# Optimization experiments

Hardware: AMD Instinct MI355X
Metric: run time of the kernel (lower is better)

The kernel has to match this reference:

```python
import jax, jax.numpy as jnp
import numpy as np

N, E, D, H, L = 50000, 800000, 64, 4, 2
DH = D // H


def layer_norm(h, g, b, eps=1e-5):
    mu = h.mean(-1, keepdims=True)
    var = ((h - mu) ** 2).mean(-1, keepdims=True)
    return (h - mu) / jnp.sqrt(var + eps) * g + b


def setup_inputs() -> dict:
    key = jax.random.key(0)
    ks = jax.random.split(key, 16)
    s = 1.0 / np.sqrt(D)
    inp = {
        "x": jax.random.normal(ks[0], (N, D), jnp.float32),
        "edge_attr": jax.random.normal(ks[1], (E, D), jnp.float32),
        "edge_index": jax.random.randint(ks[2], (2, E), 0, N, jnp.int64),
        "WQ": jax.random.normal(ks[3], (L, D, D), jnp.float32) * s,
        "WK": jax.random.normal(ks[4], (L, D, D), jnp.float32) * s,
        "WE": jax.random.normal(ks[5], (L, D, D), jnp.float32) * s,
        "WV": jax.random.normal(ks[6], (L, D, D), jnp.float32) * s,
        "WO": jax.random.normal(ks[7], (L, D, D), jnp.float32) * s,
        "bO": jnp.zeros((L, D), jnp.float32),
        "ln1_g": jnp.ones((L, D), jnp.float32),
        "ln1_b": jnp.zeros((L, D), jnp.float32),
        "W1": jax.random.normal(ks[8], (L, D, 2 * D), jnp.float32) * s,
        "b1": jnp.zeros((L, 2 * D), jnp.float32),
        "W2": jax.random.normal(ks[9], (L, 2 * D, D), jnp.float32) * (1.0 / np.sqrt(2 * D)),
        "b2": jnp.zeros((L, D), jnp.float32),
        "ln2_g": jnp.ones((L, D), jnp.float32),
        "ln2_b": jnp.zeros((L, D), jnp.float32),
    }
    return inp


def exphormer_layer(h, edge_attr, src, dst, p):
    (wq, wk, we, wv, wo, bo, g1, be1, w1, b1, w2, b2, g2, be2) = p
    n = h.shape[0]
    Qh = (h @ wq).reshape(n, H, DH)
    Kh = (h @ wk).reshape(n, H, DH)
    Vh = (h @ wv).reshape(n, H, DH)
    Eh = (edge_attr @ we).reshape(-1, H, DH)
    # per-edge score: sum over head_dim of K[src]*Q[dst]*E / sqrt(DH)
    s = jnp.sum(Kh[src] * Qh[dst] * Eh, axis=-1, keepdims=True) / np.sqrt(DH)
    score = jnp.exp(jnp.clip(s, -5.0, 5.0))  # [E, H, 1]
    msg = Vh[src] * score                     # [E, H, DH]
    wV = jax.ops.segment_sum(msg, dst, num_segments=n)    # [N, H, DH]
    Z = jax.ops.segment_sum(score, dst, num_segments=n)   # [N, H, 1]
    h_attn = (wV / (Z + 1e-6)).reshape(n, D)
    h1 = layer_norm(h + (h_attn @ wo + bo), g1, be1)
    ffn = jax.nn.relu(h1 @ w1 + b1) @ w2 + b2
    return layer_norm(h1 + ffn, g2, be2)


def reference(x, edge_attr, edge_index, WQ, WK, WE, WV, WO, bO, ln1_g, ln1_b,
              W1, b1, W2, b2, ln2_g, ln2_b):
    src = edge_index[0]
    dst = edge_index[1]
    h = x
    for l in range(L):
        p = (WQ[l], WK[l], WE[l], WV[l], WO[l], bO[l], ln1_g[l], ln1_b[l],
             W1[l], b1[l], W2[l], b2[l], ln2_g[l], ln2_b[l])
        h = exphormer_layer(h, edge_attr, src, dst, p)
    return h
```

## Files before the change

### kernel.cpp

```cpp
#include <hip/hip_runtime.h>

#define NN 50000
#define NE 800000
#define D  64
#define NL 2
#define NB 196

typedef __bf16 bf16x8 __attribute__((ext_vector_type(8)));
typedef float  floatx4 __attribute__((ext_vector_type(4)));

static __device__ __forceinline__ float bf2f(unsigned short u) {
    return __uint_as_float(((unsigned)u) << 16);
}
static __device__ __forceinline__ unsigned short f2bf(float x) {
    unsigned u = __float_as_uint(x);
    u += 0x7fff + ((u >> 16) & 1);
    return (unsigned short)(u >> 16);
}


__global__ void k_deg(const int* __restrict__ ei, int* __restrict__ deg) {
    int e = blockIdx.x * 256 + threadIdx.x;
    if (e < NE) atomicAdd(&deg[ei[NE + e]], 1);
}

__global__ __launch_bounds__(256) void k_scan1(const int* __restrict__ deg,
                                               int* __restrict__ psum) {
    __shared__ int red[4];
    int i = blockIdx.x * 256 + threadIdx.x;
    int v = (i < NN) ? deg[i] : 0;
#pragma unroll
    for (int m = 1; m < 64; m <<= 1) v += __shfl_xor(v, m, 64);
    if ((threadIdx.x & 63) == 0) red[threadIdx.x >> 6] = v;
    __syncthreads();
    if (threadIdx.x == 0) psum[blockIdx.x] = red[0] + red[1] + red[2] + red[3];
}

__global__ void k_scan2(int* __restrict__ psum) {
    __shared__ int buf[256];
    int t = threadIdx.x;
    int v = (t < NB) ? psum[t] : 0;
    buf[t] = v;
    __syncthreads();
    for (int o = 1; o < 256; o <<= 1) {
        int x = (t >= o) ? buf[t - o] : 0;
        __syncthreads();
        buf[t] += x;
        __syncthreads();
    }
    if (t < NB) psum[t] = buf[t] - v;
}

__global__ __launch_bounds__(256) void k_scan3(const int* __restrict__ deg,
                                               const int* __restrict__ psum,
                                               int* __restrict__ row_off,
                                               int* __restrict__ cursor) {
    __shared__ int buf[256];
    int t = threadIdx.x;
    int i = blockIdx.x * 256 + t;
    int v = (i < NN) ? deg[i] : 0;
    buf[t] = v;
    __syncthreads();
    for (int o = 1; o < 256; o <<= 1) {
        int x = (t >= o) ? buf[t - o] : 0;
        __syncthreads();
        buf[t] += x;
        __syncthreads();
    }
    if (i < NN) {
        int inc = buf[t] + psum[blockIdx.x];
        row_off[i + 1] = inc;
        cursor[i] = inc - v;
        if (i == 0) row_off[0] = 0;
    }
}

__global__ void k_scatter(const int* __restrict__ ei, int* __restrict__ cursor,
                          int* __restrict__ csr_src, int* __restrict__ csr_dst,
                          int* __restrict__ eperm) {
    int e = blockIdx.x * 256 + threadIdx.x;
    if (e < NE) {
        int dst = ei[NE + e];
        int pos = atomicAdd(&cursor[dst], 1);
        csr_src[pos] = ei[e];
        csr_dst[pos] = dst;
        eperm[e] = pos;
    }
}

__global__ __launch_bounds__(256) void k_prep(
        const float* __restrict__ WQ, const float* __restrict__ WK,
        const float* __restrict__ WV, const float* __restrict__ WE,
        const float* __restrict__ WO, const float* __restrict__ W1,
        const float* __restrict__ W2,
        unsigned short* __restrict__ wqT, unsigned short* __restrict__ wkT,
        unsigned short* __restrict__ wvT, unsigned short* __restrict__ weT,
        unsigned short* __restrict__ woT, unsigned short* __restrict__ w1T,
        unsigned short* __restrict__ w2T) {
    int idx = blockIdx.x * 256 + threadIdx.x;
    if (idx >= 2 * 36864) return;
    int l = idx / 36864;
    int r = idx % 36864;
    if (r < 20480) {
        int which = r >> 12, rr = r & 4095;
        int m = rr >> 6, k = rr & 63;
        const float* src = (which == 0 ? WQ : which == 1 ? WK : which == 2 ? WV :
                            which == 3 ? WE : WO);
        unsigned short* dst = (which == 0 ? wqT : which == 1 ? wkT : which == 2 ? wvT :
                               which == 3 ? weT : woT);
        dst[l * 4096 + rr] = f2bf(src[l * 4096 + k * 64 + m]);
    } else if (r < 28672) {
        int r2 = r - 20480;
        int m = r2 >> 6, k = r2 & 63;
        w1T[l * 8192 + r2] = f2bf(W1[l * 8192 + k * 128 + m]);
    } else {
        int r3 = r - 28672;
        int m = r3 >> 7, k = r3 & 127;
        w2T[l * 8192 + r3] = f2bf(W2[l * 8192 + k * 64 + m]);
    }
}


__global__ __launch_bounds__(256) void k_qkv_mfma(const float* __restrict__ h,
        const unsigned short* __restrict__ wqT, const unsigned short* __restrict__ wkT,
        const unsigned short* __restrict__ wvT,
        unsigned short* __restrict__ Qb, unsigned short* __restrict__ Kb,
        unsigned short* __restrict__ Vb) {
    __shared__ unsigned short st[4][16 * 72];
    const int lane = threadIdx.x & 63;
    const int w    = threadIdx.x >> 6;
    const int ml   = lane & 15;
    const int quad = lane >> 4;

    bf16x8 aq[2][4], ak[2][4], av[2][4];
#pragma unroll
    for (int kt = 0; kt < 2; kt++)
#pragma unroll
        for (int mt = 0; mt < 4; mt++) {
            int o = (mt*16 + ml)*64 + kt*32 + quad*8;
            aq[kt][mt] = *(const bf16x8*)&wqT[o];
            ak[kt][mt] = *(const bf16x8*)&wkT[o];
            av[kt][mt] = *(const bf16x8*)&wvT[o];
        }

    const int wave = blockIdx.x * 4 + w;
    const int nw   = gridDim.x * 4;
    const int el = lane >> 2, c = lane & 3;
    for (int tile = wave; tile < NN / 16; tile += nw) {
        const int e0 = tile * 16;
        const float4* ar = (const float4*)(h + (size_t)(e0 + ml) * D);
        bf16x8 b[2];
#pragma unroll
        for (int kt = 0; kt < 2; kt++) {
            float4 f0 = ar[kt*8 + quad*2 + 0];
            float4 f1 = ar[kt*8 + quad*2 + 1];
            b[kt][0] = (__bf16)f0.x; b[kt][1] = (__bf16)f0.y;
            b[kt][2] = (__bf16)f0.z; b[kt][3] = (__bf16)f0.w;
            b[kt][4] = (__bf16)f1.x; b[kt][5] = (__bf16)f1.y;
            b[kt][6] = (__bf16)f1.z; b[kt][7] = (__bf16)f1.w;
        }
        floatx4 accq[4] = {}, acck[4] = {}, accv[4] = {};
#pragma unroll
        for (int kt = 0; kt < 2; kt++)
#pragma unroll
            for (int mt = 0; mt < 4; mt++) {
                accq[mt] = __builtin_amdgcn_mfma_f32_16x16x32_bf16(aq[kt][mt], b[kt], accq[mt], 0, 0, 0);
                acck[mt] = __builtin_amdgcn_mfma_f32_16x16x32_bf16(ak[kt][mt], b[kt], acck[mt], 0, 0, 0);
                accv[mt] = __builtin_amdgcn_mfma_f32_16x16x32_bf16(av[kt][mt], b[kt], accv[mt], 0, 0, 0);
            }
#pragma unroll
        for (int mt = 0; mt < 4; mt++)
            *(ushort4*)&st[w][ml*72 + mt*16 + quad*4] =
                make_ushort4(f2bf(accq[mt][0]), f2bf(accq[mt][1]),
                             f2bf(accq[mt][2]), f2bf(accq[mt][3]));
        {
            uint4 r0 = *(const uint4*)&st[w][el*72 + c*16 + 0];
            uint4 r1 = *(const uint4*)&st[w][el*72 + c*16 + 8];
            uint4* gp = (uint4*)(Qb + (size_t)(e0 + el) * D + c*16);
            gp[0] = r0; gp[1] = r1;
        }
#pragma unroll
        for (int mt = 0; mt < 4; mt++)
            *(ushort4*)&st[w][ml*72 + mt*16 + quad*4] =
                make_ushort4(f2bf(acck[mt][0]), f2bf(acck[mt][1]),
                             f2bf(acck[mt][2]), f2bf(acck[mt][3]));
        {
            uint4 r0 = *(const uint4*)&st[w][el*72 + c*16 + 0];
            uint4 r1 = *(const uint4*)&st[w][el*72 + c*16 + 8];
            uint4* gp = (uint4*)(Kb + (size_t)(e0 + el) * D + c*16);
            gp[0] = r0; gp[1] = r1;
        }
#pragma unroll
        for (int mt = 0; mt < 4; mt++)
            *(ushort4*)&st[w][ml*72 + mt*16 + quad*4] =
                make_ushort4(f2bf(accv[mt][0]), f2bf(accv[mt][1]),
                             f2bf(accv[mt][2]), f2bf(accv[mt][3]));
        {
            uint4 r0 = *(const uint4*)&st[w][el*72 + c*16 + 0];
            uint4 r1 = *(const uint4*)&st[w][el*72 + c*16 + 8];
            uint4* gp = (uint4*)(Vb + (size_t)(e0 + el) * D + c*16);
            gp[0] = r0; gp[1] = r1;
        }
    }
}

__global__ __launch_bounds__(256) void k_eh_score(const float* __restrict__ ea,
        const unsigned short* __restrict__ weT, const int* __restrict__ eperm,
        const int* __restrict__ ei, const unsigned short* __restrict__ Qb,
        const unsigned short* __restrict__ Kb,
        float* __restrict__ scb, unsigned short* __restrict__ Eh1) {
    __shared__ unsigned short wsm[2 * 4608];
    __shared__ unsigned short st[4][16 * 72];
    const int t = threadIdx.x;
    for (int i = t; i < 1024; i += 256) {
        int l = i >> 9, r = i & 511;
        *(uint4*)&wsm[l*4608 + (r >> 3)*72 + (r & 7)*8] = ((const uint4*)weT)[i];
    }
    __syncthreads();

    const int lane = t & 63;
    const int w    = t >> 6;
    const int ml   = lane & 15;
    const int quad = lane >> 4;
    const int el = lane >> 2, c = lane & 3;
    const int wave = blockIdx.x * 4 + w;
    const int nw   = gridDim.x * 4;
    const int NT   = NE / 16;

    int tile = wave;
    if (tile >= NT) return;
    int srcn = ei[tile*16 + ml];
    int dstn = ei[NE + tile*16 + ml];
    int posm = eperm[tile*16 + ml];
    int pose = eperm[tile*16 + el];

    for (; tile < NT; tile += nw) {
        const float4* ar = (const float4*)(ea + (size_t)(tile*16 + ml) * D);
        float4 f00 = ar[quad*2 + 0];
        float4 f01 = ar[quad*2 + 1];
        float4 f10 = ar[8 + quad*2 + 0];
        float4 f11 = ar[8 + quad*2 + 1];
        ushort4 qg[4], kg[4];
#pragma unroll
        for (int mt = 0; mt < 4; mt++) {
            qg[mt] = *(const ushort4*)(Qb + (size_t)dstn * D + mt*16 + quad*4);
            kg[mt] = *(const ushort4*)(Kb + (size_t)srcn * D + mt*16 + quad*4);
        }
        int nxt = tile + nw;
        int nsrc = srcn, ndst = dstn, nposm = posm, npose = pose;
        if (nxt < NT) {
            nsrc  = ei[nxt*16 + ml];
            ndst  = ei[NE + nxt*16 + ml];
            nposm = eperm[nxt*16 + ml];
            npose = eperm[nxt*16 + el];
        }
        bf16x8 b[2];
        b[0][0] = (__bf16)f00.x; b[0][1] = (__bf16)f00.y;
        b[0][2] = (__bf16)f00.z; b[0][3] = (__bf16)f00.w;
        b[0][4] = (__bf16)f01.x; b[0][5] = (__bf16)f01.y;
        b[0][6] = (__bf16)f01.z; b[0][7] = (__bf16)f01.w;
        b[1][0] = (__bf16)f10.x; b[1][1] = (__bf16)f10.y;
        b[1][2] = (__bf16)f10.z; b[1][3] = (__bf16)f10.w;
        b[1][4] = (__bf16)f11.x; b[1][5] = (__bf16)f11.y;
        b[1][6] = (__bf16)f11.z; b[1][7] = (__bf16)f11.w;

        {
            floatx4 acc[4] = {};
#pragma unroll
            for (int kt = 0; kt < 2; kt++)
#pragma unroll
                for (int mt = 0; mt < 4; mt++) {
                    bf16x8 a = *(const bf16x8*)&wsm[4608 + (mt*16 + ml)*72 + kt*32 + quad*8];
                    acc[mt] = __builtin_amdgcn_mfma_f32_16x16x32_bf16(a, b[kt], acc[mt], 0, 0, 0);
                }
#pragma unroll
            for (int mt = 0; mt < 4; mt++)
                *(ushort4*)&st[w][ml*72 + mt*16 + quad*4] =
                    make_ushort4(f2bf(acc[mt][0]), f2bf(acc[mt][1]),
                                 f2bf(acc[mt][2]), f2bf(acc[mt][3]));
            uint4 r0 = *(const uint4*)&st[w][el*72 + c*16 + 0];
            uint4 r1 = *(const uint4*)&st[w][el*72 + c*16 + 8];
            uint4* gp = (uint4*)(Eh1 + (size_t)pose * D + c*16);
            gp[0] = r0;
            gp[1] = r1;
        }
        {
            floatx4 acc[4] = {};
#pragma unroll
            for (int kt = 0; kt < 2; kt++)
#pragma unroll
                for (int mt = 0; mt < 4; mt++) {
                    bf16x8 a = *(const bf16x8*)&wsm[(mt*16 + ml)*72 + kt*32 + quad*8];
                    acc[mt] = __builtin_amdgcn_mfma_f32_16x16x32_bf16(a, b[kt], acc[mt], 0, 0, 0);
                }
            float scq[4];
#pragma unroll
            for (int mt = 0; mt < 4; mt++) {
                float p = acc[mt][0] * bf2f(qg[mt].x) * bf2f(kg[mt].x)
                        + acc[mt][1] * bf2f(qg[mt].y) * bf2f(kg[mt].y)
                        + acc[mt][2] * bf2f(qg[mt].z) * bf2f(kg[mt].z)
                        + acc[mt][3] * bf2f(qg[mt].w) * bf2f(kg[mt].w);
                p += __shfl_xor(p, 16, 64);
                p += __shfl_xor(p, 32, 64);
                scq[mt] = __expf(fminf(5.f, fmaxf(-5.f, p * 0.25f)));
            }
            if (quad == 0)
                *(float4*)(scb + (size_t)posm * 4) =
                    make_float4(scq[0], scq[1], scq[2], scq[3]);
        }
        srcn = nsrc; dstn = ndst; posm = nposm; pose = npose;
    }
}

__global__ __launch_bounds__(256) void k_score1(
        const unsigned short* __restrict__ Eh1,
        const unsigned short* __restrict__ Qb, const unsigned short* __restrict__ Kb,
        const int* __restrict__ csr_src, const int* __restrict__ csr_dst,
        float* __restrict__ scb) {
    const int lane = threadIdx.x & 63;
    const int w    = threadIdx.x >> 6;
    const int ml   = lane & 15;
    const int quad = lane >> 4;
    const int wave = blockIdx.x * 4 + w;
    const int nw   = gridDim.x * 4;
    const int NT   = NE / 16;
    int tile = wave;
    if (tile >= NT) return;
    int p0 = tile*16 + ml;
    int src = csr_src[p0], dst = csr_dst[p0];
    bf16x8 e0 = *(const bf16x8*)(Eh1 + (size_t)p0 * D + quad*16);
    bf16x8 e1 = *(const bf16x8*)(Eh1 + (size_t)p0 * D + quad*16 + 8);
    for (; tile < NT; tile += nw) {
        bf16x8 k0 = *(const bf16x8*)(Kb + (size_t)src * D + quad*16);
        bf16x8 k1 = *(const bf16x8*)(Kb + (size_t)src * D + quad*16 + 8);
        bf16x8 q0 = *(const bf16x8*)(Qb + (size_t)dst * D + quad*16);
        bf16x8 q1 = *(const bf16x8*)(Qb + (size_t)dst * D + quad*16 + 8);
        int nxt = tile + nw;
        int nsrc = src, ndst = dst;
        bf16x8 ne0 = e0, ne1 = e1;
        if (nxt < NT) {
            int pn = nxt*16 + ml;
            nsrc = csr_src[pn]; ndst = csr_dst[pn];
            ne0 = *(const bf16x8*)(Eh1 + (size_t)pn * D + quad*16);
            ne1 = *(const bf16x8*)(Eh1 + (size_t)pn * D + quad*16 + 8);
        }
        float s = 0.f;
#pragma unroll
        for (int i = 0; i < 8; i++) s += (float)e0[i] * (float)q0[i] * (float)k0[i];
#pragma unroll
        for (int i = 0; i < 8; i++) s += (float)e1[i] * (float)q1[i] * (float)k1[i];
        scb[(size_t)(tile*16 + ml) * 4 + quad] = __expf(fminf(5.f, fmaxf(-5.f, s * 0.25f)));
        src = nsrc; dst = ndst; e0 = ne0; e1 = ne1;
    }
}

__global__ __launch_bounds__(256) void k_agg(
        const unsigned short* __restrict__ Vb, const float* __restrict__ scb,
        const int* __restrict__ row_off, const int* __restrict__ csr_src,
        float* __restrict__ h_attn) {
    const int node = blockIdx.x * 4 + (threadIdx.x >> 6);
    if (node >= NN) return;
    const int lane  = threadIdx.x & 63;
    const int eslot = lane >> 4;
    const int ml    = lane & 15;
    const int hsel  = ml >> 2;
    const int beg = row_off[node], end = row_off[node + 1];
    float4 acc = make_float4(0.f, 0.f, 0.f, 0.f);
    float z = 0.f;

    for (int cbeg = beg; cbeg < end; cbeg += 64) {
        const int cnt = min(64, end - cbeg);
        int myidx = cbeg + lane;
        int mysrc = (myidx < end) ? csr_src[myidx] : 0;

        for (int base = 0; base < cnt; base += 16) {
            int  jj[4];
            int  s[4];
            bool act[4];
#pragma unroll
            for (int u = 0; u < 4; u++) {
                int j = base + eslot + 4 * u;
                act[u] = j < cnt;
                jj[u]  = act[u] ? j : 0;
                s[u]   = __shfl(mysrc, jj[u], 64);
            }
            ushort4 vb[4];
            float   sv[4];
#pragma unroll
            for (int u = 0; u < 4; u++) {
                vb[u] = *(const ushort4*)(Vb + (size_t)s[u] * D + ml * 4);
                sv[u] = scb[(size_t)(cbeg + jj[u]) * 4 + hsel];
            }
#pragma unroll
            for (int u = 0; u < 4; u++) {
                float sc = act[u] ? sv[u] : 0.f;
                acc.x += sc * bf2f(vb[u].x);
                acc.y += sc * bf2f(vb[u].y);
                acc.z += sc * bf2f(vb[u].z);
                acc.w += sc * bf2f(vb[u].w);
                z += sc;
            }
        }
    }
#pragma unroll
    for (int m = 16; m <= 32; m <<= 1) {
        acc.x += __shfl_xor(acc.x, m, 64);
        acc.y += __shfl_xor(acc.y, m, 64);
        acc.z += __shfl_xor(acc.z, m, 64);
        acc.w += __shfl_xor(acc.w, m, 64);
        z     += __shfl_xor(z, m, 64);
    }
    if (eslot == 0) {
        float inv = 1.f / (z + 1e-6f);
        ((float4*)(h_attn + (size_t)node * D))[ml] =
            make_float4(acc.x * inv, acc.y * inv, acc.z * inv, acc.w * inv);
    }
}

__global__ __launch_bounds__(512) void k_post_mfma(const float* __restrict__ h_in,
        const float* __restrict__ h_attn,
        const unsigned short* __restrict__ woT_g,
        const unsigned short* __restrict__ w1T_g,
        const unsigned short* __restrict__ w2T_g,
        const float* __restrict__ bo,
        const float* __restrict__ g1, const float* __restrict__ be1,
        const float* __restrict__ b1, const float* __restrict__ b2,
        const float* __restrict__ g2, const float* __restrict__ be2,
        float* __restrict__ h_out) {
    __shared__ unsigned short woT_s[64 * 72];
    __shared__ unsigned short w1T_s[128 * 72];
    __shared__ unsigned short w2T_s[64 * 136];
    __shared__ unsigned short stg[8][16 * 136];

    const int t = threadIdx.x;
    {
        const uint4* s0 = (const uint4*)woT_g;
        { int i = t; if (i < 512) { int row = i >> 3, c = i & 7;
              *(uint4*)&woT_s[row*72 + c*8] = s0[i]; } }
        const uint4* s1 = (const uint4*)w1T_g;
        for (int i = t; i < 1024; i += 512) {
            int row = i >> 3, c = i & 7;
            *(uint4*)&w1T_s[row*72 + c*8] = s1[i];
        }
        const uint4* s2 = (const uint4*)w2T_g;
        for (int i = t; i < 1024; i += 512) {
            int row = i >> 4, c = i & 15;
            *(uint4*)&w2T_s[row*136 + c*8] = s2[i];
        }
    }
    __syncthreads();

    const int w = t >> 6, lane = t & 63;
    const int ml = lane & 15, quad = lane >> 4;
    const int tile = blockIdx.x * 8 + w;
    if (tile >= NN / 16) return;
    const int e0 = tile * 16;
    unsigned short* st = stg[w];

    const float4* ap = (const float4*)(h_attn + (size_t)(e0 + ml) * D);
    floatx4 acc1[4] = {};
#pragma unroll
    for (int kt = 0; kt < 2; kt++) {
        float4 f0 = ap[kt*8 + quad*2 + 0];
        float4 f1 = ap[kt*8 + quad*2 + 1];
        bf16x8 b;
        b[0] = (__bf16)f0.x; b[1] = (__bf16)f0.y; b[2] = (__bf16)f0.z; b[3] = (__bf16)f0.w;
        b[4] = (__bf16)f1.x; b[5] = (__bf16)f1.y; b[6] = (__bf16)f1.z; b[7] = (__bf16)f1.w;
#pragma unroll
        for (int mt = 0; mt < 4; mt++) {
            bf16x8 a = *(const bf16x8*)&woT_s[(mt*16 + ml)*72 + kt*32 + quad*8];
            acc1[mt] = __builtin_amdgcn_mfma_f32_16x16x32_bf16(a, b, acc1[mt], 0, 0, 0);
        }
    }
    const float4* hp  = (const float4*)(h_in + (size_t)(e0 + ml) * D);
    const float4* bo4 = (const float4*)bo;
    floatx4 tt[4];
#pragma unroll
    for (int mt = 0; mt < 4; mt++) {
        float4 hh = hp[mt*4 + quad];
        float4 bb = bo4[mt*4 + quad];
        tt[mt][0] = acc1[mt][0] + hh.x + bb.x;
        tt[mt][1] = acc1[mt][1] + hh.y + bb.y;
        tt[mt][2] = acc1[mt][2] + hh.z + bb.z;
        tt[mt][3] = acc1[mt][3] + hh.w + bb.w;
    }
    float s = 0.f;
#pragma unroll
    for (int mt = 0; mt < 4; mt++) s += tt[mt][0] + tt[mt][1] + tt[mt][2] + tt[mt][3];
    s += __shfl_xor(s, 16, 64); s += __shfl_xor(s, 32, 64);
    float mu = s * (1.f / 64.f);
    float v = 0.f;
#pragma unroll
    for (int mt = 0; mt < 4; mt++)
#pragma unroll
        for (int r = 0; r < 4; r++) { float c = tt[mt][r] - mu; v += c * c; }
    v += __shfl_xor(v, 16, 64); v += __shfl_xor(v, 32, 64);
    float rstd = rsqrtf(v * (1.f / 64.f) + 1e-5f);
    const float4* g1v  = (const float4*)g1;
    const float4* be1v = (const float4*)be1;
    floatx4 h1[4];
#pragma unroll
    for (int mt = 0; mt < 4; mt++) {
        float4 gg = g1v[mt*4 + quad];
        float4 bb = be1v[mt*4 + quad];
        h1[mt][0] = (tt[mt][0] - mu) * rstd * gg.x + bb.x;
        h1[mt][1] = (tt[mt][1] - mu) * rstd * gg.y + bb.y;
        h1[mt][2] = (tt[mt][2] - mu) * rstd * gg.z + bb.z;
        h1[mt][3] = (tt[mt][3] - mu) * rstd * gg.w + bb.w;
        *(ushort4*)&st[ml*136 + mt*16 + quad*4] =
            make_ushort4(f2bf(h1[mt][0]), f2bf(h1[mt][1]), f2bf(h1[mt][2]), f2bf(h1[mt][3]));
    }

    bf16x8 bh[2];
#pragma unroll
    for (int kt = 0; kt < 2; kt++)
        bh[kt] = *(const bf16x8*)&st[ml*136 + kt*32 + quad*8];
    floatx4 acc2[8] = {};
#pragma unroll
    for (int kt = 0; kt < 2; kt++)
#pragma unroll
        for (int mt = 0; mt < 8; mt++) {
            bf16x8 a = *(const bf16x8*)&w1T_s[(mt*16 + ml)*72 + kt*32 + quad*8];
            acc2[mt] = __builtin_amdgcn_mfma_f32_16x16x32_bf16(a, bh[kt], acc2[mt], 0, 0, 0);
        }
    const float4* b1v = (const float4*)b1;
#pragma unroll
    for (int mt = 0; mt < 8; mt++) {
        float4 bb = b1v[mt*4 + quad];
        float y0 = fmaxf(acc2[mt][0] + bb.x, 0.f);
        float y1 = fmaxf(acc2[mt][1] + bb.y, 0.f);
        float y2 = fmaxf(acc2[mt][2] + bb.z, 0.f);
        float y3 = fmaxf(acc2[mt][3] + bb.w, 0.f);
        *(ushort4*)&st[ml*136 + mt*16 + quad*4] =
            make_ushort4(f2bf(y0), f2bf(y1), f2bf(y2), f2bf(y3));
    }

    floatx4 acc3[4] = {};
#pragma unroll
    for (int kt = 0; kt < 4; kt++) {
        bf16x8 b = *(const bf16x8*)&st[ml*136 + kt*32 + quad*8];
#pragma unroll
        for (int mt = 0; mt < 4; mt++) {
            bf16x8 a = *(const bf16x8*)&w2T_s[(mt*16 + ml)*136 + kt*32 + quad*8];
            acc3[mt] = __builtin_amdgcn_mfma_f32_16x16x32_bf16(a, b, acc3[mt], 0, 0, 0);
        }
    }
    const float4* b2v = (const float4*)b2;
#pragma unroll
    for (int mt = 0; mt < 4; mt++) {
        float4 bb = b2v[mt*4 + quad];
        tt[mt][0] = acc3[mt][0] + bb.x + h1[mt][0];
        tt[mt][1] = acc3[mt][1] + bb.y + h1[mt][1];
        tt[mt][2] = acc3[mt][2] + bb.z + h1[mt][2];
        tt[mt][3] = acc3[mt][3] + bb.w + h1[mt][3];
    }
    s = 0.f;
#pragma unroll
    for (int mt = 0; mt < 4; mt++) s += tt[mt][0] + tt[mt][1] + tt[mt][2] + tt[mt][3];
    s += __shfl_xor(s, 16, 64); s += __shfl_xor(s, 32, 64);
    mu = s * (1.f / 64.f);
    v = 0.f;
#pragma unroll
    for (int mt = 0; mt < 4; mt++)
#pragma unroll
        for (int r = 0; r < 4; r++) { float c = tt[mt][r] - mu; v += c * c; }
    v += __shfl_xor(v, 16, 64); v += __shfl_xor(v, 32, 64);
    rstd = rsqrtf(v * (1.f / 64.f) + 1e-5f);
    const float4* g2v  = (const float4*)g2;
    const float4* be2v = (const float4*)be2;
    float4* outp = (float4*)(h_out + (size_t)(e0 + ml) * D);
#pragma unroll
    for (int mt = 0; mt < 4; mt++) {
        float4 gg = g2v[mt*4 + quad];
        float4 bb = be2v[mt*4 + quad];
        float4 o;
        o.x = (tt[mt][0] - mu) * rstd * gg.x + bb.x;
        o.y = (tt[mt][1] - mu) * rstd * gg.y + bb.y;
        o.z = (tt[mt][2] - mu) * rstd * gg.z + bb.z;
        o.w = (tt[mt][3] - mu) * rstd * gg.w + bb.w;
        outp[mt*4 + quad] = o;
    }
}


extern "C" void kernel_launch(void* const* d_in, const int* in_sizes, int n_in,
                              void* d_out, int out_size, void* d_ws, size_t ws_size,
                              hipStream_t stream) {
    const float* x   = (const float*)d_in[0];
    const float* ea  = (const float*)d_in[1];
    const int*   ei  = (const int*)d_in[2];
    const float* WQ  = (const float*)d_in[3];
    const float* WK  = (const float*)d_in[4];
    const float* WE  = (const float*)d_in[5];
    const float* WV  = (const float*)d_in[6];
    const float* WO  = (const float*)d_in[7];
    const float* bO  = (const float*)d_in[8];
    const float* g1  = (const float*)d_in[9];
    const float* be1 = (const float*)d_in[10];
    const float* W1  = (const float*)d_in[11];
    const float* b1  = (const float*)d_in[12];
    const float* W2  = (const float*)d_in[13];
    const float* b2  = (const float*)d_in[14];
    const float* g2  = (const float*)d_in[15];
    const float* be2 = (const float*)d_in[16];
    float* out = (float*)d_out;

    char* wsb = (char*)d_ws;
    size_t off = 0;
    auto alloc = [&](size_t bytes) {
        void* p = wsb + off;
        off += (bytes + 255) & ~(size_t)255;
        return p;
    };
    unsigned short* Qb   = (unsigned short*)alloc((size_t)NN * D * 2);
    unsigned short* Kb   = (unsigned short*)alloc((size_t)NN * D * 2);
    unsigned short* Vb   = (unsigned short*)alloc((size_t)NN * D * 2);
    float* hbuf          = (float*)alloc((size_t)NN * D * 4);
    float* hattn         = (float*)alloc((size_t)NN * D * 4);
    unsigned short* Eh1  = (unsigned short*)alloc((size_t)NE * D * 2);
    float* scb           = (float*)alloc((size_t)NE * 4 * 4);
    int* row_off         = (int*)alloc((size_t)(NN + 1) * 4);
    int* cursor          = (int*)alloc((size_t)NN * 4);
    int* deg             = (int*)alloc((size_t)NN * 4);
    int* psum            = (int*)alloc((size_t)256 * 4);
    int* csr_src         = (int*)alloc((size_t)NE * 4);
    int* csr_dst         = (int*)alloc((size_t)NE * 4);
    int* eperm           = (int*)alloc((size_t)NE * 4);
    unsigned short* wqT  = (unsigned short*)alloc((size_t)2 * 4096 * 2);
    unsigned short* wkT  = (unsigned short*)alloc((size_t)2 * 4096 * 2);
    unsigned short* wvT  = (unsigned short*)alloc((size_t)2 * 4096 * 2);
    unsigned short* weT  = (unsigned short*)alloc((size_t)2 * 4096 * 2);
    unsigned short* woT  = (unsigned short*)alloc((size_t)2 * 4096 * 2);
    unsigned short* w1T  = (unsigned short*)alloc((size_t)2 * 8192 * 2);
    unsigned short* w2T  = (unsigned short*)alloc((size_t)2 * 8192 * 2);

    hipMemsetAsync(deg, 0, (size_t)NN * 4, stream);
    k_deg<<<(NE + 255) / 256, 256, 0, stream>>>(ei, deg);
    k_scan1<<<NB, 256, 0, stream>>>(deg, psum);
    k_scan2<<<1, 256, 0, stream>>>(psum);
    k_scan3<<<NB, 256, 0, stream>>>(deg, psum, row_off, cursor);
    k_scatter<<<(NE + 255) / 256, 256, 0, stream>>>(ei, cursor, csr_src, csr_dst, eperm);
    k_prep<<<(2 * 36864 + 255) / 256, 256, 0, stream>>>(WQ, WK, WV, WE, WO, W1, W2,
            wqT, wkT, wvT, weT, woT, w1T, w2T);

    k_qkv_mfma<<<782, 256, 0, stream>>>(x, wqT, wkT, wvT, Qb, Kb, Vb);
    k_eh_score<<<1280, 256, 0, stream>>>(ea, weT, eperm, ei, Qb, Kb, scb, Eh1);

    k_agg<<<(NN + 3) / 4, 256, 0, stream>>>(Vb, scb, row_off, csr_src, hattn);
    k_post_mfma<<<(NN / 16 + 7) / 8, 512, 0, stream>>>(x, hattn,
            woT, w1T, w2T, bO, g1, be1, b1, b2, g2, be2, hbuf);

    k_qkv_mfma<<<782, 256, 0, stream>>>(hbuf, wqT + 4096, wkT + 4096,
                                        wvT + 4096, Qb, Kb, Vb);
    k_score1<<<1536, 256, 0, stream>>>(Eh1, Qb, Kb, csr_src, csr_dst, scb);
    k_agg<<<(NN + 3) / 4, 256, 0, stream>>>(Vb, scb, row_off, csr_src, hattn);
    k_post_mfma<<<(NN / 16 + 7) / 8, 512, 0, stream>>>(hbuf, hattn,
            woT + 4096, w1T + 8192, w2T + 8192,
            bO + 64, g1 + 64, be1 + 64, b1 + 128, b2 + 64,
            g2 + 64, be2 + 64, out);
}
```

Measured before the change: 605.8 us.

## Store edge features in original order, drop csr_dst, use bf16 h_attn

The layer-1 edge feature projection Eh1 is now written in original edge order instead of CSR-permuted order, so its stores are contiguous rather than scattered. The second-layer score kernel reads src/dst straight from edge_index and scatters only the small score values through eperm, which removes the csr_dst array and its writes in the scatter kernel. The attention output h_attn is stored as bf16 instead of fp32, halving that buffer's traffic and removing the conversion in the post kernel. The trade is scattered 16-byte score writes in place of sequential ones, plus rounding of h_attn to bf16, which the MFMA path already did.

```diff
diff --git a/kernel.cpp b/kernel.cpp
--- a/kernel.cpp
+++ b/kernel.cpp
@@ -76,14 +76,12 @@
 }
 
 __global__ void k_scatter(const int* __restrict__ ei, int* __restrict__ cursor,
-                          int* __restrict__ csr_src, int* __restrict__ csr_dst,
-                          int* __restrict__ eperm) {
+                          int* __restrict__ csr_src, int* __restrict__ eperm) {
     int e = blockIdx.x * 256 + threadIdx.x;
     if (e < NE) {
         int dst = ei[NE + e];
         int pos = atomicAdd(&cursor[dst], 1);
         csr_src[pos] = ei[e];
-        csr_dst[pos] = dst;
         eperm[e] = pos;
     }
 }
@@ -232,7 +230,6 @@
     int srcn = ei[tile*16 + ml];
     int dstn = ei[NE + tile*16 + ml];
     int posm = eperm[tile*16 + ml];
-    int pose = eperm[tile*16 + el];
 
     for (; tile < NT; tile += nw) {
         const float4* ar = (const float4*)(ea + (size_t)(tile*16 + ml) * D);
@@ -247,12 +244,11 @@
             kg[mt] = *(const ushort4*)(Kb + (size_t)srcn * D + mt*16 + quad*4);
         }
         int nxt = tile + nw;
-        int nsrc = srcn, ndst = dstn, nposm = posm, npose = pose;
+        int nsrc = srcn, ndst = dstn, nposm = posm;
         if (nxt < NT) {
             nsrc  = ei[nxt*16 + ml];
             ndst  = ei[NE + nxt*16 + ml];
             nposm = eperm[nxt*16 + ml];
-            npose = eperm[nxt*16 + el];
         }
         bf16x8 b[2];
         b[0][0] = (__bf16)f00.x; b[0][1] = (__bf16)f00.y;
@@ -280,7 +276,7 @@
                                  f2bf(acc[mt][2]), f2bf(acc[mt][3]));
             uint4 r0 = *(const uint4*)&st[w][el*72 + c*16 + 0];
             uint4 r1 = *(const uint4*)&st[w][el*72 + c*16 + 8];
-            uint4* gp = (uint4*)(Eh1 + (size_t)pose * D + c*16);
+            uint4* gp = (uint4*)(Eh1 + (size_t)(tile*16 + el) * D + c*16);
             gp[0] = r0;
             gp[1] = r1;
         }
@@ -308,14 +304,14 @@
                 *(float4*)(scb + (size_t)posm * 4) =
                     make_float4(scq[0], scq[1], scq[2], scq[3]);
         }
-        srcn = nsrc; dstn = ndst; posm = nposm; pose = npose;
+        srcn = nsrc; dstn = ndst; posm = nposm;
     }
 }
 
 __global__ __launch_bounds__(256) void k_score1(
         const unsigned short* __restrict__ Eh1,
         const unsigned short* __restrict__ Qb, const unsigned short* __restrict__ Kb,
-        const int* __restrict__ csr_src, const int* __restrict__ csr_dst,
+        const int* __restrict__ ei, const int* __restrict__ eperm,
         float* __restrict__ scb) {
     const int lane = threadIdx.x & 63;
     const int w    = threadIdx.x >> 6;
@@ -327,7 +323,7 @@
     int tile = wave;
     if (tile >= NT) return;
     int p0 = tile*16 + ml;
-    int src = csr_src[p0], dst = csr_dst[p0];
+    int src = ei[p0], dst = ei[NE + p0], pos = eperm[p0];
     bf16x8 e0 = *(const bf16x8*)(Eh1 + (size_t)p0 * D + quad*16);
     bf16x8 e1 = *(const bf16x8*)(Eh1 + (size_t)p0 * D + quad*16 + 8);
     for (; tile < NT; tile += nw) {
@@ -336,11 +332,11 @@
         bf16x8 q0 = *(const bf16x8*)(Qb + (size_t)dst * D + quad*16);
         bf16x8 q1 = *(const bf16x8*)(Qb + (size_t)dst * D + quad*16 + 8);
         int nxt = tile + nw;
-        int nsrc = src, ndst = dst;
+        int nsrc = src, ndst = dst, npos = pos;
         bf16x8 ne0 = e0, ne1 = e1;
         if (nxt < NT) {
             int pn = nxt*16 + ml;
-            nsrc = csr_src[pn]; ndst = csr_dst[pn];
+            nsrc = ei[pn]; ndst = ei[NE + pn]; npos = eperm[pn];
             ne0 = *(const bf16x8*)(Eh1 + (size_t)pn * D + quad*16);
             ne1 = *(const bf16x8*)(Eh1 + (size_t)pn * D + quad*16 + 8);
         }
@@ -349,15 +345,15 @@
         for (int i = 0; i < 8; i++) s += (float)e0[i] * (float)q0[i] * (float)k0[i];
 #pragma unroll
         for (int i = 0; i < 8; i++) s += (float)e1[i] * (float)q1[i] * (float)k1[i];
-        scb[(size_t)(tile*16 + ml) * 4 + quad] = __expf(fminf(5.f, fmaxf(-5.f, s * 0.25f)));
-        src = nsrc; dst = ndst; e0 = ne0; e1 = ne1;
+        scb[(size_t)pos * 4 + quad] = __expf(fminf(5.f, fmaxf(-5.f, s * 0.25f)));
+        src = nsrc; dst = ndst; pos = npos; e0 = ne0; e1 = ne1;
     }
 }
 
 __global__ __launch_bounds__(256) void k_agg(
         const unsigned short* __restrict__ Vb, const float* __restrict__ scb,
         const int* __restrict__ row_off, const int* __restrict__ csr_src,
-        float* __restrict__ h_attn) {
+        unsigned short* __restrict__ h_attn) {
     const int node = blockIdx.x * 4 + (threadIdx.x >> 6);
     if (node >= NN) return;
     const int lane  = threadIdx.x & 63;
@@ -412,13 +408,14 @@
     }
     if (eslot == 0) {
         float inv = 1.f / (z + 1e-6f);
-        ((float4*)(h_attn + (size_t)node * D))[ml] =
-            make_float4(acc.x * inv, acc.y * inv, acc.z * inv, acc.w * inv);
+        *(ushort4*)&h_attn[(size_t)node * D + ml * 4] =
+            make_ushort4(f2bf(acc.x * inv), f2bf(acc.y * inv),
+                         f2bf(acc.z * inv), f2bf(acc.w * inv));
     }
 }
 
 __global__ __launch_bounds__(512) void k_post_mfma(const float* __restrict__ h_in,
-        const float* __restrict__ h_attn,
+        const unsigned short* __restrict__ h_attn,
         const unsigned short* __restrict__ woT_g,
         const unsigned short* __restrict__ w1T_g,
         const unsigned short* __restrict__ w2T_g,
@@ -457,15 +454,10 @@
     const int e0 = tile * 16;
     unsigned short* st = stg[w];
 
-    const float4* ap = (const float4*)(h_attn + (size_t)(e0 + ml) * D);
     floatx4 acc1[4] = {};
 #pragma unroll
     for (int kt = 0; kt < 2; kt++) {
-        float4 f0 = ap[kt*8 + quad*2 + 0];
-        float4 f1 = ap[kt*8 + quad*2 + 1];
-        bf16x8 b;
-        b[0] = (__bf16)f0.x; b[1] = (__bf16)f0.y; b[2] = (__bf16)f0.z; b[3] = (__bf16)f0.w;
-        b[4] = (__bf16)f1.x; b[5] = (__bf16)f1.y; b[6] = (__bf16)f1.z; b[7] = (__bf16)f1.w;
+        bf16x8 b = *(const bf16x8*)(h_attn + (size_t)(e0 + ml) * D + kt*32 + quad*8);
 #pragma unroll
         for (int mt = 0; mt < 4; mt++) {
             bf16x8 a = *(const bf16x8*)&woT_s[(mt*16 + ml)*72 + kt*32 + quad*8];
@@ -616,7 +608,7 @@
     unsigned short* Kb   = (unsigned short*)alloc((size_t)NN * D * 2);
     unsigned short* Vb   = (unsigned short*)alloc((size_t)NN * D * 2);
     float* hbuf          = (float*)alloc((size_t)NN * D * 4);
-    float* hattn         = (float*)alloc((size_t)NN * D * 4);
+    unsigned short* hattn= (unsigned short*)alloc((size_t)NN * D * 2);
     unsigned short* Eh1  = (unsigned short*)alloc((size_t)NE * D * 2);
     float* scb           = (float*)alloc((size_t)NE * 4 * 4);
     int* row_off         = (int*)alloc((size_t)(NN + 1) * 4);
@@ -624,7 +616,6 @@
     int* deg             = (int*)alloc((size_t)NN * 4);
     int* psum            = (int*)alloc((size_t)256 * 4);
     int* csr_src         = (int*)alloc((size_t)NE * 4);
-    int* csr_dst         = (int*)alloc((size_t)NE * 4);
     int* eperm           = (int*)alloc((size_t)NE * 4);
     unsigned short* wqT  = (unsigned short*)alloc((size_t)2 * 4096 * 2);
     unsigned short* wkT  = (unsigned short*)alloc((size_t)2 * 4096 * 2);
@@ -639,7 +630,7 @@
     k_scan1<<<NB, 256, 0, stream>>>(deg, psum);
     k_scan2<<<1, 256, 0, stream>>>(psum);
     k_scan3<<<NB, 256, 0, stream>>>(deg, psum, row_off, cursor);
-    k_scatter<<<(NE + 255) / 256, 256, 0, stream>>>(ei, cursor, csr_src, csr_dst, eperm);
+    k_scatter<<<(NE + 255) / 256, 256, 0, stream>>>(ei, cursor, csr_src, eperm);
     k_prep<<<(2 * 36864 + 255) / 256, 256, 0, stream>>>(WQ, WK, WV, WE, WO, W1, W2,
             wqT, wkT, wvT, weT, woT, w1T, w2T);
 
@@ -652,7 +643,7 @@
 
     k_qkv_mfma<<<782, 256, 0, stream>>>(hbuf, wqT + 4096, wkT + 4096,
                                         wvT + 4096, Qb, Kb, Vb);
-    k_score1<<<1536, 256, 0, stream>>>(Eh1, Qb, Kb, csr_src, csr_dst, scb);
+    k_score1<<<1536, 256, 0, stream>>>(Eh1, Qb, Kb, ei, eperm, scb);
     k_agg<<<(NN + 3) / 4, 256, 0, stream>>>(Vb, scb, row_off, csr_src, hattn);
     k_post_mfma<<<(NN / 16 + 7) / 8, 512, 0, stream>>>(hbuf, hattn,
             woT + 4096, w1T + 8192, w2T + 8192,
```

Measured after the change: 622.2 us. 1.03x slower.
